# Performance work log

Measured on AMD Instinct MI355X. Metric: run time of the kernel, lower is better.

## Reference

```python
import jax, jax.numpy as jnp
import numpy as np

FEATURE_DIM = 768
LAMBDA_REG = 0.01
NUM_ITERS = 5
LR = 0.1
SIGMA = 2.0
MARGIN = 1.0
BN_EPS = 1e-5


def setup_inputs() -> dict:
    key = jax.random.key(0)
    ks = jax.random.split(key, 10)
    B, D = 32, FEATURE_DIM
    search_features = jax.random.normal(ks[0], (B, D, 32, 32), dtype=jnp.float32)
    target_features = jax.random.normal(ks[1], (B, D, 16, 16), dtype=jnp.float32)
    target_mask = jax.random.uniform(ks[2], (B, 1, 16, 16), dtype=jnp.float32)
    conv_w = jax.random.normal(ks[3], (D, D), dtype=jnp.float32) * (1.0 / np.sqrt(D))
    conv_b = jax.random.normal(ks[4], (D,), dtype=jnp.float32) * 0.01
    bn_gamma = jnp.ones((D,), dtype=jnp.float32)
    bn_beta = jnp.zeros((D,), dtype=jnp.float32)
    bn_mean = jax.random.normal(ks[5], (D,), dtype=jnp.float32) * 0.01
    bn_var = jax.random.uniform(ks[6], (D,), dtype=jnp.float32, minval=0.5, maxval=1.5)
    filter_init = jax.random.normal(ks[7], (1, D, 1, 1), dtype=jnp.float32) * 0.01
    return {
        "search_features": search_features,
        "target_features": target_features,
        "target_mask": target_mask,
        "conv_w": conv_w,
        "conv_b": conv_b,
        "bn_gamma": bn_gamma,
        "bn_beta": bn_beta,
        "bn_mean": bn_mean,
        "bn_var": bn_var,
        "filter_init": filter_init,
    }


def _proj(x, conv_w, conv_b, bn_gamma, bn_beta, bn_mean, bn_var):
    # 1x1 conv == channel-wise GEMM, then BatchNorm (eval mode, running stats)
    y = jnp.einsum('bdhw,ed->behw', x, conv_w) + conv_b[None, :, None, None]
    inv_std = bn_gamma / jnp.sqrt(bn_var + BN_EPS)
    return (y - bn_mean[None, :, None, None]) * inv_std[None, :, None, None] + bn_beta[None, :, None, None]


def _gaussian_label(mask):
    B, _, H, W = mask.shape
    yy, xx = jnp.meshgrid(jnp.arange(H, dtype=jnp.float32), jnp.arange(W, dtype=jnp.float32), indexing='ij')
    yy = yy[None, None]  # (1,1,H,W)
    xx = xx[None, None]
    msum = jnp.clip(mask.sum(axis=(2, 3), keepdims=True), 1.0)
    cy = (mask * yy).sum(axis=(2, 3), keepdims=True) / msum
    cx = (mask * xx).sum(axis=(2, 3), keepdims=True) / msum
    return jnp.exp(-((xx - cx) ** 2 + (yy - cy) ** 2) / (2.0 * SIGMA ** 2))


def reference(search_features, target_features, target_mask, conv_w, conv_b,
              bn_gamma, bn_beta, bn_mean, bn_var, filter_init):
    sp = _proj(search_features, conv_w, conv_b, bn_gamma, bn_beta, bn_mean, bn_var)
    tp = _proj(target_features, conv_w, conv_b, bn_gamma, bn_beta, bn_mean, bn_var)
    B = tp.shape[0]
    label = _gaussian_label(target_mask)  # (B,1,H',W')
    f = jnp.broadcast_to(filter_init, (B,) + filter_init.shape[1:])  # (B,D,1,1)
    for _ in range(NUM_ITERS):
        response = (tp * f).sum(axis=1, keepdims=True)  # (B,1,H',W')
        loss = jnp.maximum(MARGIN - response * label, 0.0)
        grad = jnp.where(loss > 0, -label * target_mask, 0.0)
        grad = grad.mean(axis=(2, 3), keepdims=True)  # (B,1,1,1), broadcasts over D
        f = f - LR * (grad + LAMBDA_REG * f)
    return (sp * f).sum(axis=1, keepdims=True)  # (B,1,H,W)
```

## Files before the change

### kernel.cpp

```cpp
#include <hip/hip_runtime.h>
#include <math.h>

#define DD   768
#define BB   32
#define NTP  256
#define NSP  1024
#define NT   (BB*NTP)
#define NS   (BB*NSP)
#define ECH  16
#define CHE  (DD/ECH)
#define NO   8
#define OCH  (DD/NO)

#define OFF_UP  0
#define OFF_VP  (OFF_UP + ECH*DD)
#define OFF_K   (OFF_VP + ECH*DD)
#define OFF_TR0 (OFF_K + 64)
#define OFF_TS0 (OFF_TR0 + NO*NT)
#define OFF_SR  (OFF_TS0 + NO*NT)
#define OFF_SS  (OFF_SR + NO*NS)

#define A5 0.99500999000499900f

__global__ void k_prep(const float* __restrict__ w, const float* __restrict__ cb,
                       const float* __restrict__ gamma, const float* __restrict__ beta,
                       const float* __restrict__ mean, const float* __restrict__ var,
                       const float* __restrict__ fi, float* __restrict__ ws) {
    int bx = blockIdx.x;
    int t = threadIdx.x;
    if (bx < ECH) {
        __shared__ float wu[CHE], wv[CHE];
        if (t < CHE) {
            int e = bx * CHE + t;
            float inv = gamma[e] / sqrtf(var[e] + 1e-5f);
            wv[t] = inv;
            wu[t] = inv * fi[e];
        }
        __syncthreads();
        if (t < 192) {
            const float4* w4 = (const float4*)w;
            float4 Ru = {0,0,0,0}, Rv = {0,0,0,0};
            #pragma unroll
            for (int j = 0; j < CHE; ++j) {
                float4 x = w4[(size_t)(bx * CHE + j) * 192 + t];
                float a = wu[j], b = wv[j];
                Ru.x += x.x * a; Ru.y += x.y * a; Ru.z += x.z * a; Ru.w += x.w * a;
                Rv.x += x.x * b; Rv.y += x.y * b; Rv.z += x.z * b; Rv.w += x.w * b;
            }
            *(float4*)(ws + OFF_UP + bx * DD + t * 4) = Ru;
            *(float4*)(ws + OFF_VP + bx * DD + t * 4) = Rv;
        }
    } else {
        __shared__ float r1[256], r2[256];
        float a1 = 0.f, a2 = 0.f;
        for (int e = t; e < DD; e += 256) {
            float inv = gamma[e] / sqrtf(var[e] + 1e-5f);
            float x = (cb[e] - mean[e]) * inv + beta[e];
            a1 += x * fi[e];
            a2 += x;
        }
        r1[t] = a1; r2[t] = a2;
        __syncthreads();
        for (int s = 128; s > 0; s >>= 1) {
            if (t < s) { r1[t] += r1[t + s]; r2[t] += r2[t + s]; }
            __syncthreads();
        }
        if (t == 0) { ws[OFF_K] = r1[0]; ws[OFF_K + 1] = r2[0]; }
    }
}

__global__ __launch_bounds__(256, 5) void k_big(const float* __restrict__ sf,
                                                const float* __restrict__ tf,
                                                float* __restrict__ ws) {
    int bx = blockIdx.x;
    int t = threadIdx.x;
    int pxf4 = t & 63, sub = t >> 6;

    int b, q, oct; bool isS;
    if (bx < 1024) { isS = true;  oct = bx & 7; q = (bx >> 3) & 3; b = bx >> 5; }
    else           { isS = false; int u = bx - 1024; oct = u & 7; q = 0; b = u >> 3; }

    __shared__ float su[OCH], sv[OCH];
    if (t < 24) {
        float4 U = {0,0,0,0};
        #pragma unroll
        for (int ec = 0; ec < ECH; ++ec) {
            float4 a = ((const float4*)(ws + OFF_UP))[ec * 192 + oct * 24 + t];
            U.x += a.x; U.y += a.y; U.z += a.z; U.w += a.w;
        }
        ((float4*)su)[t] = U;
    } else if (t < 48) {
        int j = t - 24;
        float4 V = {0,0,0,0};
        #pragma unroll
        for (int ec = 0; ec < ECH; ++ec) {
            float4 c = ((const float4*)(ws + OFF_VP))[ec * 192 + oct * 24 + j];
            V.x += c.x; V.y += c.y; V.z += c.z; V.w += c.w;
        }
        ((float4*)sv)[j] = V;
    }
    __syncthreads();

    const float4* base;
    int STR;
    float4 *oR, *oS;
    if (isS) {
        base = (const float4*)sf + ((size_t)b * DD + oct * OCH + sub * 24) * (NSP/4) + q * 64 + pxf4;
        STR = NSP / 4;
        int g4 = b * 256 + q * 64 + pxf4;
        oR = (float4*)(ws + OFF_SR) + oct * (NS/4) + g4;
        oS = (float4*)(ws + OFF_SS) + oct * (NS/4) + g4;
    } else {
        base = (const float4*)tf + ((size_t)b * DD + oct * OCH + sub * 24) * (NTP/4) + pxf4;
        STR = NTP / 4;
        int g4 = b * 64 + pxf4;
        oR = (float4*)(ws + OFF_TR0) + oct * (NT/4) + g4;
        oS = (float4*)(ws + OFF_TS0) + oct * (NT/4) + g4;
    }

    float4 accR = {0,0,0,0}, accS = {0,0,0,0};
    float4 buf[12];
    #pragma unroll
    for (int k = 0; k < 12; ++k) buf[k] = base[(size_t)k * STR];
    #pragma unroll
    for (int i = 0; i < 24; ++i) {
        float4 v = buf[i % 12];
        if (i < 12) buf[i % 12] = base[(size_t)(i + 12) * STR];
        float u = su[sub * 24 + i], vb = sv[sub * 24 + i];
        accR.x += v.x * u;  accR.y += v.y * u;  accR.z += v.z * u;  accR.w += v.w * u;
        accS.x += v.x * vb; accS.y += v.y * vb; accS.z += v.z * vb; accS.w += v.w * vb;
    }

    __shared__ float4 redR[4][64], redS[4][64];
    redR[sub][pxf4] = accR; redS[sub][pxf4] = accS;
    __syncthreads();
    if (sub < 2) {
        float4 a = redR[sub + 2][pxf4], m = redR[sub][pxf4];
        m.x += a.x; m.y += a.y; m.z += a.z; m.w += a.w; redR[sub][pxf4] = m;
        float4 c = redS[sub + 2][pxf4], n = redS[sub][pxf4];
        n.x += c.x; n.y += c.y; n.z += c.z; n.w += c.w; redS[sub][pxf4] = n;
    }
    __syncthreads();
    if (sub == 0) {
        float4 a = redR[1][pxf4], m = redR[0][pxf4];
        m.x += a.x; m.y += a.y; m.z += a.z; m.w += a.w;
        float4 c = redS[1][pxf4], n = redS[0][pxf4];
        n.x += c.x; n.y += c.y; n.z += c.z; n.w += c.w;
        *oR = m; *oS = n;
    }
}

__global__ void k_final(const float* __restrict__ mask, const float* __restrict__ ws,
                        float* __restrict__ out) {
    int b = blockIdx.x;
    int p = threadIdx.x;
    int lane = p & 63, wv = p >> 6;
    int h = p >> 4, w = p & 15;
    float K1 = ws[OFF_K], K2 = ws[OFF_K + 1];
    float r0 = K1, s0 = K2;
    #pragma unroll
    for (int o = 0; o < NO; ++o) {
        r0 += ws[OFF_TR0 + o * NT + b * 256 + p];
        s0 += ws[OFF_TS0 + o * NT + b * 256 + p];
    }
    float m = mask[b * 256 + p];
    __shared__ float cross[4];
    auto bsum = [&](float v) -> float {
        #pragma unroll
        for (int o = 32; o > 0; o >>= 1) v += __shfl_xor(v, o, 64);
        if (lane == 0) cross[wv] = v;
        __syncthreads();
        float r = cross[0] + cross[1] + cross[2] + cross[3];
        __syncthreads();
        return r;
    };
    float msum = bsum(m);
    float sy = bsum(m * (float)h);
    float sx = bsum(m * (float)w);
    msum = fmaxf(msum, 1.0f);
    float cy = sy / msum, cx = sx / msum;
    float dx = (float)w - cx, dy = (float)h - cy;
    float label = expf(-(dx * dx + dy * dy) * 0.125f);
    float A = 1.0f, c = 0.0f;
    const float decay = 1.0f - 0.1f * 0.01f;
    #pragma unroll
    for (int it = 0; it < 5; ++it) {
        float resp = A * r0 + c * s0;
        float gc = (1.0f - resp * label > 0.0f) ? (-label * m) : 0.0f;
        float g = bsum(gc) * (1.0f / 256.0f);
        c = decay * c - 0.1f * g;
        A *= decay;
    }
    int g4 = b * 256 + p;
    float4 R = {K1, K1, K1, K1}, S = {K2, K2, K2, K2};
    #pragma unroll
    for (int o = 0; o < NO; ++o) {
        float4 a = ((const float4*)(ws + OFF_SR))[o * (NS/4) + g4];
        float4 d = ((const float4*)(ws + OFF_SS))[o * (NS/4) + g4];
        R.x += a.x; R.y += a.y; R.z += a.z; R.w += a.w;
        S.x += d.x; S.y += d.y; S.z += d.z; S.w += d.w;
    }
    float4 o;
    o.x = A5 * R.x + c * S.x;
    o.y = A5 * R.y + c * S.y;
    o.z = A5 * R.z + c * S.z;
    o.w = A5 * R.w + c * S.w;
    ((float4*)out)[g4] = o;
}

extern "C" void kernel_launch(void* const* d_in, const int* in_sizes, int n_in,
                              void* d_out, int out_size, void* d_ws, size_t ws_size,
                              hipStream_t stream) {
    const float* sf    = (const float*)d_in[0];
    const float* tf    = (const float*)d_in[1];
    const float* mask  = (const float*)d_in[2];
    const float* w     = (const float*)d_in[3];
    const float* cb    = (const float*)d_in[4];
    const float* gamma = (const float*)d_in[5];
    const float* beta  = (const float*)d_in[6];
    const float* mean  = (const float*)d_in[7];
    const float* var   = (const float*)d_in[8];
    const float* fi    = (const float*)d_in[9];
    float* out = (float*)d_out;
    float* ws  = (float*)d_ws;

    k_prep <<<ECH + 1, 256, 0, stream>>>(w, cb, gamma, beta, mean, var, fi, ws);
    k_big  <<<1280,    256, 0, stream>>>(sf, tf, ws);
    k_final<<<BB,      256, 0, stream>>>(mask, ws, out);
}
```

Measured before the change: 35.14 us.

## Reshape projection-reduction grid into fewer blocks with longer per-thread channel loops

Result: slower. 36.26 us (+3.2%).

```diff
diff --git a/kernel.cpp b/kernel.cpp
--- a/kernel.cpp
+++ b/kernel.cpp
@@ -7,18 +7,18 @@
 #define NSP  1024
 #define NT   (BB*NTP)
 #define NS   (BB*NSP)
-#define ECH  16
+#define ECH  32
 #define CHE  (DD/ECH)
-#define NO   8
-#define OCH  (DD/NO)
+#define NSL  8
+#define NTL  2
 
 #define OFF_UP  0
 #define OFF_VP  (OFF_UP + ECH*DD)
 #define OFF_K   (OFF_VP + ECH*DD)
 #define OFF_TR0 (OFF_K + 64)
-#define OFF_TS0 (OFF_TR0 + NO*NT)
-#define OFF_SR  (OFF_TS0 + NO*NT)
-#define OFF_SS  (OFF_SR + NO*NS)
+#define OFF_TS0 (OFF_TR0 + NTL*NT)
+#define OFF_SR  (OFF_TS0 + NTL*NT)
+#define OFF_SS  (OFF_SR + NSL*NS)
 
 #define A5 0.99500999000499900f
 
@@ -69,84 +69,106 @@
     }
 }
 
-__global__ __launch_bounds__(256, 5) void k_big(const float* __restrict__ sf,
-                                                const float* __restrict__ tf,
-                                                float* __restrict__ ws) {
+__global__ __launch_bounds__(256) void k_big(const float* __restrict__ sf,
+                                             const float* __restrict__ tf,
+                                             float* __restrict__ ws) {
     int bx = blockIdx.x;
     int t = threadIdx.x;
-    int pxf4 = t & 63, sub = t >> 6;
-
-    int b, q, oct; bool isS;
-    if (bx < 1024) { isS = true;  oct = bx & 7; q = (bx >> 3) & 3; b = bx >> 5; }
-    else           { isS = false; int u = bx - 1024; oct = u & 7; q = 0; b = u >> 3; }
-
-    __shared__ float su[OCH], sv[OCH];
-    if (t < 24) {
-        float4 U = {0,0,0,0};
-        #pragma unroll
-        for (int ec = 0; ec < ECH; ++ec) {
-            float4 a = ((const float4*)(ws + OFF_UP))[ec * 192 + oct * 24 + t];
-            U.x += a.x; U.y += a.y; U.z += a.z; U.w += a.w;
-        }
-        ((float4*)su)[t] = U;
-    } else if (t < 48) {
-        int j = t - 24;
-        float4 V = {0,0,0,0};
-        #pragma unroll
-        for (int ec = 0; ec < ECH; ++ec) {
-            float4 c = ((const float4*)(ws + OFF_VP))[ec * 192 + oct * 24 + j];
-            V.x += c.x; V.y += c.y; V.z += c.z; V.w += c.w;
-        }
-        ((float4*)sv)[j] = V;
+    bool isS = bx < 256;
+    int b, slice;
+    if (isS) { b = bx >> 3; slice = bx & 7; }
+    else     { int u = bx - 256; b = u >> 1; slice = u & 1; }
+
+    __shared__ float su[384], sv[384];
+    if (isS) {
+        if (t < 24) {
+            float4 U = {0,0,0,0};
+            #pragma unroll
+            for (int ec = 0; ec < ECH; ++ec) {
+                float4 a = ((const float4*)(ws + OFF_UP))[ec * 192 + slice * 24 + t];
+                U.x += a.x; U.y += a.y; U.z += a.z; U.w += a.w;
+            }
+            ((float4*)su)[t] = U;
+        } else if (t < 48) {
+            int j = t - 24;
+            float4 V = {0,0,0,0};
+            #pragma unroll
+            for (int ec = 0; ec < ECH; ++ec) {
+                float4 c = ((const float4*)(ws + OFF_VP))[ec * 192 + slice * 24 + j];
+                V.x += c.x; V.y += c.y; V.z += c.z; V.w += c.w;
+            }
+            ((float4*)sv)[j] = V;
+        }
+    } else {
+        if (t < 96) {
+            float4 U = {0,0,0,0};
+            #pragma unroll
+            for (int ec = 0; ec < ECH; ++ec) {
+                float4 a = ((const float4*)(ws + OFF_UP))[ec * 192 + slice * 96 + t];
+                U.x += a.x; U.y += a.y; U.z += a.z; U.w += a.w;
+            }
+            ((float4*)su)[t] = U;
+        } else if (t < 192) {
+            int j = t - 96;
+            float4 V = {0,0,0,0};
+            #pragma unroll
+            for (int ec = 0; ec < ECH; ++ec) {
+                float4 c = ((const float4*)(ws + OFF_VP))[ec * 192 + slice * 96 + j];
+                V.x += c.x; V.y += c.y; V.z += c.z; V.w += c.w;
+            }
+            ((float4*)sv)[j] = V;
+        }
     }
     __syncthreads();
 
-    const float4* base;
-    int STR;
-    float4 *oR, *oS;
+    float4 accR = {0,0,0,0}, accS = {0,0,0,0};
     if (isS) {
-        base = (const float4*)sf + ((size_t)b * DD + oct * OCH + sub * 24) * (NSP/4) + q * 64 + pxf4;
-        STR = NSP / 4;
-        int g4 = b * 256 + q * 64 + pxf4;
-        oR = (float4*)(ws + OFF_SR) + oct * (NS/4) + g4;
-        oS = (float4*)(ws + OFF_SS) + oct * (NS/4) + g4;
+        const float4* base = (const float4*)sf + ((size_t)b * DD + slice * 96) * (NSP/4) + t;
+        float4 buf[12];
+        #pragma unroll
+        for (int k = 0; k < 12; ++k) buf[k] = base[(size_t)k * 256];
+        #pragma unroll
+        for (int i = 0; i < 96; ++i) {
+            float4 v = buf[i % 12];
+            if (i < 84) buf[i % 12] = base[(size_t)(i + 12) * 256];
+            float u = su[i], vb = sv[i];
+            accR.x += v.x * u;  accR.y += v.y * u;  accR.z += v.z * u;  accR.w += v.w * u;
+            accS.x += v.x * vb; accS.y += v.y * vb; accS.z += v.z * vb; accS.w += v.w * vb;
+        }
+        ((float4*)(ws + OFF_SR))[slice * (NS/4) + b * 256 + t] = accR;
+        ((float4*)(ws + OFF_SS))[slice * (NS/4) + b * 256 + t] = accS;
     } else {
-        base = (const float4*)tf + ((size_t)b * DD + oct * OCH + sub * 24) * (NTP/4) + pxf4;
-        STR = NTP / 4;
-        int g4 = b * 64 + pxf4;
-        oR = (float4*)(ws + OFF_TR0) + oct * (NT/4) + g4;
-        oS = (float4*)(ws + OFF_TS0) + oct * (NT/4) + g4;
-    }
-
-    float4 accR = {0,0,0,0}, accS = {0,0,0,0};
-    float4 buf[12];
-    #pragma unroll
-    for (int k = 0; k < 12; ++k) buf[k] = base[(size_t)k * STR];
-    #pragma unroll
-    for (int i = 0; i < 24; ++i) {
-        float4 v = buf[i % 12];
-        if (i < 12) buf[i % 12] = base[(size_t)(i + 12) * STR];
-        float u = su[sub * 24 + i], vb = sv[sub * 24 + i];
-        accR.x += v.x * u;  accR.y += v.y * u;  accR.z += v.z * u;  accR.w += v.w * u;
-        accS.x += v.x * vb; accS.y += v.y * vb; accS.z += v.z * vb; accS.w += v.w * vb;
-    }
-
-    __shared__ float4 redR[4][64], redS[4][64];
-    redR[sub][pxf4] = accR; redS[sub][pxf4] = accS;
-    __syncthreads();
-    if (sub < 2) {
-        float4 a = redR[sub + 2][pxf4], m = redR[sub][pxf4];
-        m.x += a.x; m.y += a.y; m.z += a.z; m.w += a.w; redR[sub][pxf4] = m;
-        float4 c = redS[sub + 2][pxf4], n = redS[sub][pxf4];
-        n.x += c.x; n.y += c.y; n.z += c.z; n.w += c.w; redS[sub][pxf4] = n;
-    }
-    __syncthreads();
-    if (sub == 0) {
-        float4 a = redR[1][pxf4], m = redR[0][pxf4];
-        m.x += a.x; m.y += a.y; m.z += a.z; m.w += a.w;
-        float4 c = redS[1][pxf4], n = redS[0][pxf4];
-        n.x += c.x; n.y += c.y; n.z += c.z; n.w += c.w;
-        *oR = m; *oS = n;
+        int f = t & 63, cg = t >> 6;
+        const float4* base = (const float4*)tf + ((size_t)b * DD + slice * 384) * (NTP/4) + t;
+        float4 buf[12];
+        #pragma unroll
+        for (int k = 0; k < 12; ++k) buf[k] = base[(size_t)k * 256];
+        #pragma unroll
+        for (int i = 0; i < 96; ++i) {
+            float4 v = buf[i % 12];
+            if (i < 84) buf[i % 12] = base[(size_t)(i + 12) * 256];
+            float u = su[cg + 4 * i], vb = sv[cg + 4 * i];
+            accR.x += v.x * u;  accR.y += v.y * u;  accR.z += v.z * u;  accR.w += v.w * u;
+            accS.x += v.x * vb; accS.y += v.y * vb; accS.z += v.z * vb; accS.w += v.w * vb;
+        }
+        __shared__ float4 redR[4][64], redS[4][64];
+        redR[cg][f] = accR; redS[cg][f] = accS;
+        __syncthreads();
+        if (cg < 2) {
+            float4 a = redR[cg + 2][f], m = redR[cg][f];
+            m.x += a.x; m.y += a.y; m.z += a.z; m.w += a.w; redR[cg][f] = m;
+            float4 c = redS[cg + 2][f], n = redS[cg][f];
+            n.x += c.x; n.y += c.y; n.z += c.z; n.w += c.w; redS[cg][f] = n;
+        }
+        __syncthreads();
+        if (cg == 0) {
+            float4 a = redR[1][f], m = redR[0][f];
+            m.x += a.x; m.y += a.y; m.z += a.z; m.w += a.w;
+            float4 c = redS[1][f], n = redS[0][f];
+            n.x += c.x; n.y += c.y; n.z += c.z; n.w += c.w;
+            ((float4*)(ws + OFF_TR0))[slice * (NT/4) + b * 64 + f] = m;
+            ((float4*)(ws + OFF_TS0))[slice * (NT/4) + b * 64 + f] = n;
+        }
     }
 }
 
@@ -157,12 +179,8 @@
     int lane = p & 63, wv = p >> 6;
     int h = p >> 4, w = p & 15;
     float K1 = ws[OFF_K], K2 = ws[OFF_K + 1];
-    float r0 = K1, s0 = K2;
-    #pragma unroll
-    for (int o = 0; o < NO; ++o) {
-        r0 += ws[OFF_TR0 + o * NT + b * 256 + p];
-        s0 += ws[OFF_TS0 + o * NT + b * 256 + p];
-    }
+    float r0 = K1 + ws[OFF_TR0 + b * 256 + p] + ws[OFF_TR0 + NT + b * 256 + p];
+    float s0 = K2 + ws[OFF_TS0 + b * 256 + p] + ws[OFF_TS0 + NT + b * 256 + p];
     float m = mask[b * 256 + p];
     __shared__ float cross[4];
     auto bsum = [&](float v) -> float {
@@ -194,7 +212,7 @@
     int g4 = b * 256 + p;
     float4 R = {K1, K1, K1, K1}, S = {K2, K2, K2, K2};
     #pragma unroll
-    for (int o = 0; o < NO; ++o) {
+    for (int o = 0; o < NSL; ++o) {
         float4 a = ((const float4*)(ws + OFF_SR))[o * (NS/4) + g4];
         float4 d = ((const float4*)(ws + OFF_SS))[o * (NS/4) + g4];
         R.x += a.x; R.y += a.y; R.z += a.z; R.w += a.w;
@@ -225,6 +243,6 @@
     float* ws  = (float*)d_ws;
 
     k_prep <<<ECH + 1, 256, 0, stream>>>(w, cb, gamma, beta, mean, var, fi, ws);
-    k_big  <<<1280,    256, 0, stream>>>(sf, tf, ws);
+    k_big  <<<320,     256, 0, stream>>>(sf, tf, ws);
     k_final<<<BB,      256, 0, stream>>>(mask, ws, out);
 }
```
